# Kernel optimization log

Measured on AMD Instinct MI355X. Metric: run time of the kernel, lower is better.

The kernel has to match this reference:

```python
import jax, jax.numpy as jnp
import numpy as np

SPLINE_ORDER = 3
TOP_K = 2
NUM_EXPERTS = 8


def _gram_basis(x, beta_w):
    # x: (B, C, H, W) post-tanh. Returns (B, C*(S+1), H, W).
    P0 = jnp.ones_like(x)
    P1 = x
    ps = [P0, P1]
    for i in range(2, SPLINE_ORDER + 1):
        n, m = i - 1, i
        # beta(n, m) = (m+n)*(m-n)*n^2 / (m^2/(4n^2-1)) * beta_weights[n]
        beta = (m + n) * (m - n) * (n ** 2) * (4.0 * n ** 2 - 1.0) / (m ** 2) * beta_w[n]
        P2 = x * ps[-1] - beta * ps[-2]
        ps.append(P2)
    return jnp.concatenate(ps, axis=1)


def _expert(x, poly_w, beta_w):
    # tanh -> Gram polynomial basis -> SiLU -> conv2d (padding=1, stride=1)
    g = jax.nn.silu(_gram_basis(jnp.tanh(x), beta_w))
    return jax.lax.conv_general_dilated(
        g, poly_w[0], window_strides=(1, 1), padding=[(1, 1), (1, 1)],
        dimension_numbers=('NCHW', 'OIHW', 'NCHW'))


def _cv_squared(v):
    # torch.var is unbiased (ddof=1)
    return jnp.var(v, ddof=1) / (jnp.mean(v) ** 2 + 1e-10)


def reference(x, w_gate, poly_weights, beta_weights):
    B = x.shape[0]
    # gating input: global average pool -> (B, C)
    gate_x = jnp.mean(x, axis=(2, 3))
    probs = jax.nn.softmax(gate_x @ w_gate, axis=1)  # softmax BEFORE topk, as in source
    top_vals, top_idx = jax.lax.top_k(probs, TOP_K + 1)
    tk_vals = top_vals[:, :TOP_K]
    tk_idx = top_idx[:, :TOP_K]
    tk_gates = tk_vals / (jnp.sum(tk_vals, axis=1, keepdims=True) + 1e-6)
    gates = jnp.zeros_like(probs).at[jnp.arange(B)[:, None], tk_idx].set(tk_gates)
    importance = gates.sum(axis=0)
    load = jnp.sum(gates > 0, axis=0).astype(jnp.float32)  # eval-mode load
    loss = (_cv_squared(importance) + _cv_squared(load)) * 0.01
    # All experts share parameters (ModuleList([experts]*num_experts)), so
    # sum_e gates[b,e] * expert_e(x[b]) == gates.sum(1)[b] * expert(x[b]).
    y = _expert(x, poly_weights, beta_weights) * jnp.sum(gates, axis=1)[:, None, None, None]
    return y, loss


def setup_inputs() -> dict:
    key = jax.random.key(0)
    k1, k2, k3, k4 = jax.random.split(key, 4)
    x = jax.random.normal(k1, (16, 32, 192, 192), dtype=jnp.float32)
    w_gate = jax.random.normal(k2, (32, NUM_EXPERTS), dtype=jnp.float32) * 0.1
    poly_weights = jax.random.normal(k3, (1, 32, 32 * (SPLINE_ORDER + 1), 3, 3), dtype=jnp.float32) * 0.05
    beta_weights = jax.random.normal(k4, (SPLINE_ORDER + 1,), dtype=jnp.float32) * 0.01
    return {"x": x, "w_gate": w_gate, "poly_weights": poly_weights, "beta_weights": beta_weights}
```

## Files before the change

kernel.cpp:

```cpp
#include <hip/hip_runtime.h>

typedef unsigned short u16;
typedef unsigned int u32;
typedef __attribute__((ext_vector_type(8))) short bf16x8;
typedef __attribute__((ext_vector_type(4))) float f32x4;

static constexpr int B = 16, C = 32, H = 192, W = 192;
static constexpr int HW = H * W;
static constexpr int E = 8;
static constexpr int CO = 32;
static constexpr long long NTOT = (long long)B * C * HW;
static constexpr float SILU1 = 0.7310585786300049f;

static constexpr size_t GX_OFF = (size_t)NTOT * 2;
static constexpr size_t SK_OFF = GX_OFF + 512 * 4;
static constexpr size_t SS_OFF = SK_OFF + 288 * 4;
static constexpr size_t WF_OFF = SS_OFF + 128;

__device__ inline u16 f2b(float f) {
    u32 u = __float_as_uint(f);
    return (u16)((u + 0x7fffu + ((u >> 16) & 1u)) >> 16);
}
__device__ inline float silu(float z) { return z / (1.0f + __expf(-z)); }

__global__ __launch_bounds__(256) void stage1_prep(const float* __restrict__ x,
                                                   const float* __restrict__ pw,
                                                   u16* __restrict__ t_out,
                                                   float* __restrict__ gate_x,
                                                   float* __restrict__ Sk,
                                                   float* __restrict__ Ssum,
                                                   u16* __restrict__ wfrag) {
    const int blk = blockIdx.x, t = threadIdx.x;
    __shared__ float sred[9][32][8];
    if (blk < 512) {
        const float4* xp = (const float4*)(x + (size_t)blk * HW);
        ushort4* tp = (ushort4*)(t_out + (size_t)blk * HW);
        float s = 0.0f;
        for (int i = t; i < HW / 4; i += 256) {
            float4 v = xp[i];
            s += (v.x + v.y) + (v.z + v.w);
            ushort4 o;
            o.x = f2b(tanhf(v.x)); o.y = f2b(tanhf(v.y));
            o.z = f2b(tanhf(v.z)); o.w = f2b(tanhf(v.w));
            tp[i] = o;
        }
        #pragma unroll
        for (int off = 32; off > 0; off >>= 1) s += __shfl_down(s, off, 64);
        if ((t & 63) == 0) sred[0][0][t >> 6] = s;
        __syncthreads();
        if (t == 0)
            gate_x[blk] = (sred[0][0][0] + sred[0][0][1] + sred[0][0][2] + sred[0][0][3])
                          * (1.0f / HW);
        return;
    }
    if (blk < 620) {
        int j = (blk - 512) * 256 + t;
        int e = j & 7, lane = (j >> 3) & 63, rest = j >> 9;
        int half = rest & 1, pt = rest >> 1;
        int p = pt / 9, tap = pt - p * 9;
        int co = half * 16 + (lane & 15);
        int ci = 32 + p * 32 + (lane >> 4) * 8 + e;
        wfrag[j] = f2b(pw[(size_t)co * 1152 + ci * 9 + tap]);
        return;
    }
    {
        const int co = t & 31, sub = t >> 5;
        #pragma unroll
        for (int k = 0; k < 9; ++k) {
            float s = 0.0f;
            #pragma unroll
            for (int i = 0; i < 4; ++i)
                s += pw[(size_t)co * 1152 + (sub * 4 + i) * 9 + k];
            sred[k][co][sub] = s;
        }
        __syncthreads();
        __shared__ float sks[288];
        for (int j = t; j < 288; j += 256) {
            int k = j >> 5, c = j & 31;
            float s = 0.0f;
            #pragma unroll
            for (int u = 0; u < 8; ++u) s += sred[k][c][u];
            sks[j] = s; Sk[j] = s;
        }
        __syncthreads();
        if (t < 32) {
            float s = 0.0f;
            #pragma unroll
            for (int k = 0; k < 9; ++k) s += sks[k * 32 + t];
            Ssum[t] = s;
        }
    }
}

static constexpr int GSTR = 40;

__global__ __launch_bounds__(256) void conv_mfma(const u16* __restrict__ t_ws,
                                                 const u16* __restrict__ wfrag,
                                                 const float* __restrict__ beta_w,
                                                 const float* __restrict__ gate_x,
                                                 const float* __restrict__ wg,
                                                 const float* __restrict__ Sk,
                                                 const float* __restrict__ Ssum,
                                                 float* __restrict__ out) {
    __shared__ __align__(16) u16 gtile[324 * GSTR];
    __shared__ float lg[B][E];
    __shared__ float scl[B];

    const int b = blockIdx.z;
    const int gx0 = blockIdx.x << 4, gy0 = blockIdx.y << 4;
    const int tid = threadIdx.x;
    const int w = tid >> 6, lane = tid & 63, q = lane >> 4, ml = lane & 15;
    const float beta2 = 2.25f * beta_w[1];
    const float beta23 = beta2 + (300.0f / 9.0f) * beta_w[2];

    const int p0 = tid;
    int extra = -1;
    if ((tid & 3) == 0) extra = tid >> 2;
    else if ((tid & 63) == 1) extra = 64 + (tid >> 6);
    const int p1 = (extra >= 0) ? 256 + extra : -1;

    u32 pk0[16], pk1[16];
    bool v0, v1 = false;
    {
        int py = p0 / 18, px = p0 - py * 18;
        int gy = gy0 + py - 1, gx = gx0 + px - 1;
        v0 = (unsigned)gy < (unsigned)H && (unsigned)gx < (unsigned)W;
        #pragma unroll
        for (int cc = 0; cc < 16; ++cc) pk0[cc] = 0u;
        if (v0) {
            const u16* tp = t_ws + (size_t)b * C * HW + gy * W + gx;
            #pragma unroll
            for (int cc = 0; cc < 16; ++cc) {
                u32 lo = tp[(size_t)(2 * cc) * HW];
                u32 hi = tp[(size_t)(2 * cc + 1) * HW];
                pk0[cc] = lo | (hi << 16);
            }
        }
        #pragma unroll
        for (int cc = 0; cc < 16; ++cc) pk1[cc] = 0u;
        if (p1 >= 0) {
            int py1 = p1 / 18, px1 = p1 - py1 * 18;
            int gy1 = gy0 + py1 - 1, gx1 = gx0 + px1 - 1;
            v1 = (unsigned)gy1 < (unsigned)H && (unsigned)gx1 < (unsigned)W;
            if (v1) {
                const u16* tp = t_ws + (size_t)b * C * HW + gy1 * W + gx1;
                #pragma unroll
                for (int cc = 0; cc < 16; ++cc) {
                    u32 lo = tp[(size_t)(2 * cc) * HW];
                    u32 hi = tp[(size_t)(2 * cc + 1) * HW];
                    pk1[cc] = lo | (hi << 16);
                }
            }
        }
    }

    if (tid < 128) {
        int gb = tid >> 3, ge = tid & 7;
        float s = 0.0f;
        #pragma unroll
        for (int c = 0; c < 32; ++c) s += gate_x[gb * 32 + c] * wg[c * 8 + ge];
        lg[gb][ge] = s;
    }
    __syncthreads();
    if (tid < 16) {
        float p[E];
        float m = lg[tid][0];
        #pragma unroll
        for (int e = 1; e < E; ++e) m = fmaxf(m, lg[tid][e]);
        float sum = 0.0f;
        #pragma unroll
        for (int e = 0; e < E; ++e) { p[e] = __expf(lg[tid][e] - m); sum += p[e]; }
        float inv = 1.0f / sum;
        #pragma unroll
        for (int e = 0; e < E; ++e) p[e] *= inv;
        int i0 = 0; float v0g = p[0];
        #pragma unroll
        for (int e = 1; e < E; ++e) if (p[e] > v0g) { v0g = p[e]; i0 = e; }
        int i1 = -1; float v1g = -1.0f;
        #pragma unroll
        for (int e = 0; e < E; ++e) { if (e == i0) continue; if (p[e] > v1g) { v1g = p[e]; i1 = e; } }
        const float denom = v0g + v1g + 1e-6f;
        const float g0 = v0g / denom, g1 = v1g / denom;
        #pragma unroll
        for (int e = 0; e < E; ++e) lg[tid][e] = 0.0f;
        lg[tid][i0] = g0; lg[tid][i1] = g1;
        scl[tid] = g0 + g1;
    }
    __syncthreads();
    if (blockIdx.x == 0 && blockIdx.y == 0 && b == 0 && tid == 0) {
        float imp[E], ld[E];
        #pragma unroll
        for (int e = 0; e < E; ++e) { imp[e] = 0.0f; ld[e] = 0.0f; }
        for (int bb = 0; bb < B; ++bb)
            #pragma unroll
            for (int e = 0; e < E; ++e) {
                float g = lg[bb][e];
                imp[e] += g;
                if (g > 0.0f) ld[e] += 1.0f;
            }
        float mi = 0.0f, mld = 0.0f;
        #pragma unroll
        for (int e = 0; e < E; ++e) { mi += imp[e]; mld += ld[e]; }
        mi *= (1.0f / E); mld *= (1.0f / E);
        float vi = 0.0f, vl = 0.0f;
        #pragma unroll
        for (int e = 0; e < E; ++e) {
            float di = imp[e] - mi, dl = ld[e] - mld;
            vi += di * di; vl += dl * dl;
        }
        vi *= (1.0f / (E - 1)); vl *= (1.0f / (E - 1));
        out[NTOT] = (vi / (mi * mi + 1e-10f) + vl / (mld * mld + 1e-10f)) * 0.01f;
    }

    f32x4 acc[4][2];
    #pragma unroll
    for (int a = 0; a < 4; ++a) {
        acc[a][0] = (f32x4){0.0f, 0.0f, 0.0f, 0.0f};
        acc[a][1] = (f32x4){0.0f, 0.0f, 0.0f, 0.0f};
    }

    #pragma unroll
    for (int p = 0; p < 3; ++p) {
        if (p) __syncthreads();
        #pragma unroll
        for (int slot = 0; slot < 2; ++slot) {
            const int pix = slot ? p1 : p0;
            if (slot && p1 < 0) continue;
            const bool vv = slot ? v1 : v0;
            const u32* pk = slot ? pk1 : pk0;
            u32 r[16];
            if (vv) {
                #pragma unroll
                for (int cc = 0; cc < 16; ++cc) {
                    float tl = __uint_as_float(pk[cc] << 16);
                    float th = __uint_as_float(pk[cc] & 0xffff0000u);
                    float ul, uh;
                    if (p == 0) { ul = tl; uh = th; }
                    else if (p == 1) { ul = fmaf(tl, tl, -beta2); uh = fmaf(th, th, -beta2); }
                    else { ul = tl * fmaf(tl, tl, -beta23); uh = th * fmaf(th, th, -beta23); }
                    u32 gl = __float_as_uint(silu(ul)) + 0x8000u;
                    u32 gh = __float_as_uint(silu(uh)) + 0x8000u;
                    r[cc] = (gl >> 16) | (gh & 0xffff0000u);
                }
            } else {
                #pragma unroll
                for (int cc = 0; cc < 16; ++cc) r[cc] = 0u;
            }
            uint4* dst = (uint4*)&gtile[pix * GSTR];
            dst[0] = *(const uint4*)&r[0];
            dst[1] = *(const uint4*)&r[4];
            dst[2] = *(const uint4*)&r[8];
            dst[3] = *(const uint4*)&r[12];
        }
        __syncthreads();
        const u16* wf = wfrag + (size_t)p * 9216;
        #pragma unroll
        for (int dx = 0; dx < 3; ++dx) {
            bf16x8 bf[3][2];
            #pragma unroll
            for (int dyi = 0; dyi < 3; ++dyi) {
                const int tap = dyi * 3 + dx;
                bf[dyi][0] = *(const bf16x8*)(wf + ((size_t)(tap * 2 + 0) * 64 + lane) * 8);
                bf[dyi][1] = *(const bf16x8*)(wf + ((size_t)(tap * 2 + 1) * 64 + lane) * 8);
            }
            #pragma unroll
            for (int rl = 0; rl < 6; ++rl) {
                const bf16x8 af = *(const bf16x8*)
                    &gtile[(((w << 2) + rl) * 18 + ml + dx) * GSTR + (q << 3)];
                #pragma unroll
                for (int dyi = 0; dyi < 3; ++dyi) {
                    const int a = rl - dyi;
                    if (a >= 0 && a < 4) {
                        acc[a][0] = __builtin_amdgcn_mfma_f32_16x16x32_bf16(af, bf[dyi][0], acc[a][0], 0, 0, 0);
                        acc[a][1] = __builtin_amdgcn_mfma_f32_16x16x32_bf16(af, bf[dyi][1], acc[a][1], 0, 0, 0);
                    }
                }
            }
        }
    }

    const float sc = scl[b];
    const bool interior = (blockIdx.x > 0) && (blockIdx.x < 11) &&
                          (blockIdx.y > 0) && (blockIdx.y < 11);
    #pragma unroll
    for (int half = 0; half < 2; ++half) {
        const int co = half * 16 + ml;
        const float bfull = SILU1 * Ssum[co];
        #pragma unroll
        for (int a = 0; a < 4; ++a) {
            const int y = gy0 + (w << 2) + a;
            float ov[4];
            #pragma unroll
            for (int r = 0; r < 4; ++r) {
                float bias = bfull;
                if (!interior) {
                    const int xg = gx0 + (q << 2) + r;
                    bias = 0.0f;
                    #pragma unroll
                    for (int k = 0; k < 9; ++k) {
                        int yy = y + k / 3 - 1, xx = xg + k % 3 - 1;
                        if ((unsigned)yy < (unsigned)H && (unsigned)xx < (unsigned)W)
                            bias += Sk[k * 32 + co];
                    }
                    bias *= SILU1;
                }
                ov[r] = (acc[a][half][r] + bias) * sc;
            }
            *(float4*)&out[((size_t)(b * CO + co) * H + y) * W + gx0 + (q << 2)] = *(float4*)ov;
        }
    }
}

extern "C" void kernel_launch(void* const* d_in, const int* in_sizes, int n_in,
                              void* d_out, int out_size, void* d_ws, size_t ws_size,
                              hipStream_t stream) {
    const float* x  = (const float*)d_in[0];
    const float* wg = (const float*)d_in[1];
    const float* pw = (const float*)d_in[2];
    const float* bw = (const float*)d_in[3];
    float* out = (float*)d_out;
    char* ws = (char*)d_ws;
    u16*   t_ws   = (u16*)ws;
    float* gate_x = (float*)(ws + GX_OFF);
    float* Sk     = (float*)(ws + SK_OFF);
    float* Ssum   = (float*)(ws + SS_OFF);
    u16*   wfrag  = (u16*)(ws + WF_OFF);

    stage1_prep<<<dim3(621), 256, 0, stream>>>(x, pw, t_ws, gate_x, Sk, Ssum, wfrag);
    conv_mfma<<<dim3(12, 12, B), 256, 0, stream>>>(t_ws, wfrag, bw, gate_x, wg, Sk, Ssum, out);
}
```

Before: 292.2 us.

## Store tanh intermediate channel-last and stage all three polynomial tiles at once

Stage1 now writes the bf16 tanh intermediate in pixel-major layout (32 channels contiguous per pixel). The conv kernel can then gather each halo pixel with four 16-byte loads instead of 32 strided 2-byte loads. The gate mean is reduced per row with atomics, tanh is replaced by an exp-based approximation, and the weight prep moves into its own kernel. The conv kernel builds all three SiLU basis tiles in a triple-size LDS buffer with one barrier, removing the per-polynomial barriers at the cost of three times the LDS, which may lower occupancy.

New measurement: 301.2 us. +3.1%, slower.

```diff
diff --git a/kernel.cpp b/kernel.cpp
--- a/kernel.cpp
+++ b/kernel.cpp
@@ -22,39 +22,50 @@
     return (u16)((u + 0x7fffu + ((u >> 16) & 1u)) >> 16);
 }
 __device__ inline float silu(float z) { return z / (1.0f + __expf(-z)); }
-
-__global__ __launch_bounds__(256) void stage1_prep(const float* __restrict__ x,
-                                                   const float* __restrict__ pw,
-                                                   u16* __restrict__ t_out,
-                                                   float* __restrict__ gate_x,
-                                                   float* __restrict__ Sk,
-                                                   float* __restrict__ Ssum,
-                                                   u16* __restrict__ wfrag) {
+__device__ inline float fast_tanh(float v) {
+    return 1.0f - 2.0f / (__expf(2.0f * v) + 1.0f);
+}
+
+__global__ void init_gate(float* __restrict__ gate_x) {
+    gate_x[threadIdx.x] = 0.0f;
+}
+
+__global__ __launch_bounds__(192) void stage1(const float* __restrict__ x,
+                                              u16* __restrict__ t_out,
+                                              float* __restrict__ gate_x) {
+    const int y = blockIdx.x, b = blockIdx.y, tx = threadIdx.x;
+    const int lane = tx & 63, wv = tx >> 6;
+    __shared__ float gred[32][3];
+    u32 pk[16];
+    #pragma unroll
+    for (int cg = 0; cg < 16; ++cg) {
+        float v0 = x[((size_t)(b * C + 2 * cg) * H + y) * W + tx];
+        float v1 = x[((size_t)(b * C + 2 * cg + 1) * H + y) * W + tx];
+        pk[cg] = (u32)f2b(fast_tanh(v0)) | ((u32)f2b(fast_tanh(v1)) << 16);
+        float s0 = v0, s1 = v1;
+        #pragma unroll
+        for (int off = 32; off > 0; off >>= 1) {
+            s0 += __shfl_down(s0, off, 64);
+            s1 += __shfl_down(s1, off, 64);
+        }
+        if (lane == 0) { gred[2 * cg][wv] = s0; gred[2 * cg + 1][wv] = s1; }
+    }
+    uint4* o = (uint4*)(t_out + ((size_t)b * HW + (size_t)y * W + tx) * 32);
+    const uint4* s4 = (const uint4*)pk;
+    o[0] = s4[0]; o[1] = s4[1]; o[2] = s4[2]; o[3] = s4[3];
+    __syncthreads();
+    if (tx < 32)
+        atomicAdd(&gate_x[b * C + tx],
+                  (gred[tx][0] + gred[tx][1] + gred[tx][2]) * (1.0f / HW));
+}
+
+__global__ __launch_bounds__(256) void prep(const float* __restrict__ pw,
+                                            float* __restrict__ Sk,
+                                            float* __restrict__ Ssum,
+                                            u16* __restrict__ wfrag) {
     const int blk = blockIdx.x, t = threadIdx.x;
-    __shared__ float sred[9][32][8];
-    if (blk < 512) {
-        const float4* xp = (const float4*)(x + (size_t)blk * HW);
-        ushort4* tp = (ushort4*)(t_out + (size_t)blk * HW);
-        float s = 0.0f;
-        for (int i = t; i < HW / 4; i += 256) {
-            float4 v = xp[i];
-            s += (v.x + v.y) + (v.z + v.w);
-            ushort4 o;
-            o.x = f2b(tanhf(v.x)); o.y = f2b(tanhf(v.y));
-            o.z = f2b(tanhf(v.z)); o.w = f2b(tanhf(v.w));
-            tp[i] = o;
-        }
-        #pragma unroll
-        for (int off = 32; off > 0; off >>= 1) s += __shfl_down(s, off, 64);
-        if ((t & 63) == 0) sred[0][0][t >> 6] = s;
-        __syncthreads();
-        if (t == 0)
-            gate_x[blk] = (sred[0][0][0] + sred[0][0][1] + sred[0][0][2] + sred[0][0][3])
-                          * (1.0f / HW);
-        return;
-    }
-    if (blk < 620) {
-        int j = (blk - 512) * 256 + t;
+    if (blk < 108) {
+        int j = blk * 256 + t;
         int e = j & 7, lane = (j >> 3) & 63, rest = j >> 9;
         int half = rest & 1, pt = rest >> 1;
         int p = pt / 9, tap = pt - p * 9;
@@ -63,32 +74,31 @@
         wfrag[j] = f2b(pw[(size_t)co * 1152 + ci * 9 + tap]);
         return;
     }
-    {
-        const int co = t & 31, sub = t >> 5;
-        #pragma unroll
-        for (int k = 0; k < 9; ++k) {
-            float s = 0.0f;
-            #pragma unroll
-            for (int i = 0; i < 4; ++i)
-                s += pw[(size_t)co * 1152 + (sub * 4 + i) * 9 + k];
-            sred[k][co][sub] = s;
-        }
-        __syncthreads();
-        __shared__ float sks[288];
-        for (int j = t; j < 288; j += 256) {
-            int k = j >> 5, c = j & 31;
-            float s = 0.0f;
-            #pragma unroll
-            for (int u = 0; u < 8; ++u) s += sred[k][c][u];
-            sks[j] = s; Sk[j] = s;
-        }
-        __syncthreads();
-        if (t < 32) {
-            float s = 0.0f;
-            #pragma unroll
-            for (int k = 0; k < 9; ++k) s += sks[k * 32 + t];
-            Ssum[t] = s;
-        }
+    __shared__ float sred[9][32][8];
+    __shared__ float sks[288];
+    const int co = t & 31, sub = t >> 5;
+    #pragma unroll
+    for (int k = 0; k < 9; ++k) {
+        float s = 0.0f;
+        #pragma unroll
+        for (int i = 0; i < 4; ++i)
+            s += pw[(size_t)co * 1152 + (sub * 4 + i) * 9 + k];
+        sred[k][co][sub] = s;
+    }
+    __syncthreads();
+    for (int j = t; j < 288; j += 256) {
+        int k = j >> 5, c = j & 31;
+        float s = 0.0f;
+        #pragma unroll
+        for (int u = 0; u < 8; ++u) s += sred[k][c][u];
+        sks[j] = s; Sk[j] = s;
+    }
+    __syncthreads();
+    if (t < 32) {
+        float s = 0.0f;
+        #pragma unroll
+        for (int k = 0; k < 9; ++k) s += sks[k * 32 + t];
+        Ssum[t] = s;
     }
 }
 
@@ -102,7 +112,7 @@
                                                  const float* __restrict__ Sk,
                                                  const float* __restrict__ Ssum,
                                                  float* __restrict__ out) {
-    __shared__ __align__(16) u16 gtile[324 * GSTR];
+    __shared__ __align__(16) u16 gtile[3][324 * GSTR];
     __shared__ float lg[B][E];
     __shared__ float scl[B];
 
@@ -120,36 +130,32 @@
     const int p1 = (extra >= 0) ? 256 + extra : -1;
 
     u32 pk0[16], pk1[16];
-    bool v0, v1 = false;
+    bool vv0, vv1 = false;
     {
         int py = p0 / 18, px = p0 - py * 18;
         int gy = gy0 + py - 1, gx = gx0 + px - 1;
-        v0 = (unsigned)gy < (unsigned)H && (unsigned)gx < (unsigned)W;
-        #pragma unroll
-        for (int cc = 0; cc < 16; ++cc) pk0[cc] = 0u;
-        if (v0) {
-            const u16* tp = t_ws + (size_t)b * C * HW + gy * W + gx;
-            #pragma unroll
-            for (int cc = 0; cc < 16; ++cc) {
-                u32 lo = tp[(size_t)(2 * cc) * HW];
-                u32 hi = tp[(size_t)(2 * cc + 1) * HW];
-                pk0[cc] = lo | (hi << 16);
-            }
-        }
-        #pragma unroll
-        for (int cc = 0; cc < 16; ++cc) pk1[cc] = 0u;
+        vv0 = (unsigned)gy < (unsigned)H && (unsigned)gx < (unsigned)W;
+        if (vv0) {
+            const uint4* tp = (const uint4*)(t_ws + ((size_t)b * HW + (size_t)gy * W + gx) * 32);
+            uint4 a0 = tp[0], a1 = tp[1], a2 = tp[2], a3 = tp[3];
+            *(uint4*)&pk0[0] = a0; *(uint4*)&pk0[4] = a1;
+            *(uint4*)&pk0[8] = a2; *(uint4*)&pk0[12] = a3;
+        } else {
+            #pragma unroll
+            for (int cc = 0; cc < 16; ++cc) pk0[cc] = 0u;
+        }
         if (p1 >= 0) {
             int py1 = p1 / 18, px1 = p1 - py1 * 18;
             int gy1 = gy0 + py1 - 1, gx1 = gx0 + px1 - 1;
-            v1 = (unsigned)gy1 < (unsigned)H && (unsigned)gx1 < (unsigned)W;
-            if (v1) {
-                const u16* tp = t_ws + (size_t)b * C * HW + gy1 * W + gx1;
+            vv1 = (unsigned)gy1 < (unsigned)H && (unsigned)gx1 < (unsigned)W;
+            if (vv1) {
+                const uint4* tp = (const uint4*)(t_ws + ((size_t)b * HW + (size_t)gy1 * W + gx1) * 32);
+                uint4 a0 = tp[0], a1 = tp[1], a2 = tp[2], a3 = tp[3];
+                *(uint4*)&pk1[0] = a0; *(uint4*)&pk1[4] = a1;
+                *(uint4*)&pk1[8] = a2; *(uint4*)&pk1[12] = a3;
+            } else {
                 #pragma unroll
-                for (int cc = 0; cc < 16; ++cc) {
-                    u32 lo = tp[(size_t)(2 * cc) * HW];
-                    u32 hi = tp[(size_t)(2 * cc + 1) * HW];
-                    pk1[cc] = lo | (hi << 16);
-                }
+                for (int cc = 0; cc < 16; ++cc) pk1[cc] = 0u;
             }
         }
     }
@@ -212,22 +218,14 @@
         out[NTOT] = (vi / (mi * mi + 1e-10f) + vl / (mld * mld + 1e-10f)) * 0.01f;
     }
 
-    f32x4 acc[4][2];
-    #pragma unroll
-    for (int a = 0; a < 4; ++a) {
-        acc[a][0] = (f32x4){0.0f, 0.0f, 0.0f, 0.0f};
-        acc[a][1] = (f32x4){0.0f, 0.0f, 0.0f, 0.0f};
-    }
-
-    #pragma unroll
-    for (int p = 0; p < 3; ++p) {
-        if (p) __syncthreads();
-        #pragma unroll
-        for (int slot = 0; slot < 2; ++slot) {
-            const int pix = slot ? p1 : p0;
-            if (slot && p1 < 0) continue;
-            const bool vv = slot ? v1 : v0;
-            const u32* pk = slot ? pk1 : pk0;
+    #pragma unroll
+    for (int slot = 0; slot < 2; ++slot) {
+        if (slot && p1 < 0) continue;
+        const int pix = slot ? p1 : p0;
+        const bool vv = slot ? vv1 : vv0;
+        const u32* pk = slot ? pk1 : pk0;
+        #pragma unroll
+        for (int p = 0; p < 3; ++p) {
             u32 r[16];
             if (vv) {
                 #pragma unroll
@@ -246,13 +244,23 @@
                 #pragma unroll
                 for (int cc = 0; cc < 16; ++cc) r[cc] = 0u;
             }
-            uint4* dst = (uint4*)&gtile[pix * GSTR];
+            uint4* dst = (uint4*)&gtile[p][pix * GSTR];
             dst[0] = *(const uint4*)&r[0];
             dst[1] = *(const uint4*)&r[4];
             dst[2] = *(const uint4*)&r[8];
             dst[3] = *(const uint4*)&r[12];
         }
-        __syncthreads();
+    }
+    __syncthreads();
+
+    f32x4 acc[4][2];
+    #pragma unroll
+    for (int a = 0; a < 4; ++a) {
+        acc[a][0] = (f32x4){0.0f, 0.0f, 0.0f, 0.0f};
+        acc[a][1] = (f32x4){0.0f, 0.0f, 0.0f, 0.0f};
+    }
+    #pragma unroll
+    for (int p = 0; p < 3; ++p) {
         const u16* wf = wfrag + (size_t)p * 9216;
         #pragma unroll
         for (int dx = 0; dx < 3; ++dx) {
@@ -266,7 +274,7 @@
             #pragma unroll
             for (int rl = 0; rl < 6; ++rl) {
                 const bf16x8 af = *(const bf16x8*)
-                    &gtile[(((w << 2) + rl) * 18 + ml + dx) * GSTR + (q << 3)];
+                    &gtile[p][(((w << 2) + rl) * 18 + ml + dx) * GSTR + (q << 3)];
                 #pragma unroll
                 for (int dyi = 0; dyi < 3; ++dyi) {
                     const int a = rl - dyi;
@@ -326,6 +334,8 @@
     float* Ssum   = (float*)(ws + SS_OFF);
     u16*   wfrag  = (u16*)(ws + WF_OFF);
 
-    stage1_prep<<<dim3(621), 256, 0, stream>>>(x, pw, t_ws, gate_x, Sk, Ssum, wfrag);
+    init_gate<<<dim3(1), 512, 0, stream>>>(gate_x);
+    stage1<<<dim3(H, B), 192, 0, stream>>>(x, t_ws, gate_x);
+    prep<<<dim3(109), 256, 0, stream>>>(pw, Sk, Ssum, wfrag);
     conv_mfma<<<dim3(12, 12, B), 256, 0, stream>>>(t_ws, wfrag, bw, gate_x, wg, Sk, Ssum, out);
 }
```
